# Optimization experiments

Hardware: AMD Instinct MI355X
Metric: run time of the kernel (lower is better)

## Reference

```python
import jax, jax.numpy as jnp
import numpy as np

HIDDEN_DIM = 256
NLAT, NLON = 64, 128
BATCH, N_STATIONS = 2, 1024


def _grid_coords():
    lat = jnp.linspace(-90.0, 90.0, NLAT)
    lon = jnp.linspace(-180.0, 180.0, NLON)
    lat_mesh, lon_mesh = jnp.meshgrid(lat, lon, indexing='ij')
    return lat_mesh.reshape(-1), lon_mesh.reshape(-1)  # (n_grid,)


def setup_inputs() -> dict:
    key = jax.random.key(0)
    k1, k2, k3, k4, k5, k6 = jax.random.split(key, 6)
    station_features = jax.random.normal(k1, (BATCH, N_STATIONS, HIDDEN_DIM), dtype=jnp.float32)
    station_coords = jax.random.normal(k2, (BATCH, N_STATIONS, 3), dtype=jnp.float32)
    mask = jnp.ones((BATCH, N_STATIONS), dtype=jnp.float32)
    # distance_mlp params: Linear(3,32) -> GELU -> Linear(32,1) -> Softplus
    W1 = jax.random.normal(k3, (3, 32), dtype=jnp.float32) * (1.0 / np.sqrt(3.0))
    b1 = jax.random.normal(k4, (32,), dtype=jnp.float32) * 0.02
    W2 = jax.random.normal(k5, (32, 1), dtype=jnp.float32) * (1.0 / np.sqrt(32.0))
    b2 = jax.random.normal(k6, (1,), dtype=jnp.float32) * 0.02
    return {"station_features": station_features, "station_coords": station_coords,
            "mask": mask, "W1": W1, "b1": b1, "W2": W2, "b2": b2}


def reference(station_features, station_coords, mask, W1, b1, W2, b2):
    lat_grid, lon_grid = _grid_coords()  # (G,)
    station_lat = station_coords[:, :, 0]  # (B,S)
    station_lon = station_coords[:, :, 1]
    dlat = station_lat[:, :, None] - lat_grid[None, None, :]  # (B,S,G)
    dlon = station_lon[:, :, None] - lon_grid[None, None, :]
    dist = jnp.sqrt(dlat**2 + dlon**2 + 1e-6)
    dist_features = jnp.stack([dist, dlat, dlon], axis=-1)  # (B,S,G,3)
    h = jax.nn.gelu(dist_features @ W1 + b1, approximate=False)  # (B,S,G,32)
    weights = jax.nn.softplus((h @ W2 + b2)[..., 0])  # (B,S,G)
    weights = weights * mask[:, :, None]
    weights = jax.nn.softmax(weights, axis=1)  # over stations
    grid = jnp.einsum('bsg,bsd->bgd', weights, station_features)
    grid = grid.reshape(station_features.shape[0], NLAT, NLON, HIDDEN_DIM)
    return jnp.transpose(grid, (0, 3, 1, 2))  # (B, D, nlat, nlon)
```

## Files before the change

### kernel.cpp

```cpp
#include <hip/hip_runtime.h>
#include <math.h>

#define NLAT 64
#define NLON 128
#define HID  256
#define NSTA 1024
#define NG   (NLAT * NLON)
#define TG   16
#define SC   128
#define NCH  4
#define NGRP 16
#define TABN 2048
#define TABW 4.5f

#define LOG2E 1.4426950408889634f
#define LN2   0.69314718055994531f

typedef float f32x4 __attribute__((ext_vector_type(4)));
typedef _Float16 f16x8 __attribute__((ext_vector_type(8)));

__device__ __forceinline__ float gelu_ref(float x) {
    const float p  = 0.3275911f;
    const float a1 = 0.254829592f, a2 = -0.284496736f, a3 = 1.421413741f,
                a4 = -1.453152027f, a5 = 1.061405429f;
    float z  = x * 0.70710678118654752f;
    float az = fabsf(z);
    float t  = __builtin_amdgcn_rcpf(fmaf(p, az, 1.0f));
    float poly = fmaf(fmaf(fmaf(fmaf(a5, t, a4), t, a3), t, a2), t, a1) * t;
    float e  = __builtin_amdgcn_exp2f(az * az * -LOG2E);
    float r  = fmaf(-poly, e, 1.0f);
    float erfz = copysignf(r, z);
    float hx = 0.5f * x;
    return fmaf(hx, erfz, hx);
}

__global__ __launch_bounds__(256)
void cvt_kernel(const float* __restrict__ feats,
                const float* __restrict__ W1, const float* __restrict__ b1,
                const float* __restrict__ W2, const float* __restrict__ b2p,
                _Float16* __restrict__ fhi, _Float16* __restrict__ flo,
                float* __restrict__ wbuf) {
    const int blk = blockIdx.x;
    if (blk == 256) {
        if (threadIdx.x == 0) {
            const float ISCALE = (float)TABN / TABW;
            const float CELL   = TABW / (float)TABN;
            float A = 0.0f, B = 0.0f, C = 0.0f, D = b2p[0];
            for (int j = 0; j < 32; ++j) {
                float a = W1[j], b = W1[32 + j], c = W1[64 + j], d = b1[j], w2 = W2[j];
                wbuf[j * 8 + 0] = a * ISCALE;
                wbuf[j * 8 + 1] = b * ISCALE;
                wbuf[j * 8 + 2] = c * ISCALE;
                wbuf[j * 8 + 3] = d * ISCALE;
                wbuf[j * 8 + 4] = w2;
                wbuf[j * 8 + 5] = 0.5f * w2 * CELL;
                wbuf[j * 8 + 6] = 0.0f;
                wbuf[j * 8 + 7] = 0.0f;
                A = fmaf(0.5f * w2, a, A);
                B = fmaf(0.5f * w2, b, B);
                C = fmaf(0.5f * w2, c, C);
                D = fmaf(0.5f * w2, d, D);
            }
            wbuf[256] = A; wbuf[257] = B; wbuf[258] = C; wbuf[259] = D;
        }
        return;
    }
    __shared__ float tile[32][68];
    const int b  = blk >> 7;
    const int st = (blk >> 2) & 31;
    const int dt = blk & 3;
    {
        const int s  = threadIdx.x >> 3;
        const int dq = threadIdx.x & 7;
        const float* src = feats + ((size_t)(b * NSTA + st * 32 + s)) * HID + dt * 64 + dq * 8;
        float4 v0 = *(const float4*)src;
        float4 v1 = *(const float4*)(src + 4);
        *(float4*)&tile[s][dq * 8]     = v0;
        *(float4*)&tile[s][dq * 8 + 4] = v1;
    }
    __syncthreads();
    const int d  = threadIdx.x >> 2;
    const int sq = threadIdx.x & 3;
    f16x8 hi8, lo8;
#pragma unroll
    for (int k = 0; k < 8; ++k) {
        float v = tile[sq * 8 + k][d];
        _Float16 h = (_Float16)v;
        hi8[k] = h;
        lo8[k] = (_Float16)(v - (float)h);
    }
    const size_t o = ((size_t)(b * HID + dt * 64 + d)) * NSTA + st * 32 + sq * 8;
    *(f16x8*)&fhi[o] = hi8;
    *(f16x8*)&flo[o] = lo8;
}

__global__ __launch_bounds__(256, 6)
void s2g_kernel(const float* __restrict__ coords,
                const float* __restrict__ maskp,
                const float* __restrict__ wbuf,
                const _Float16* __restrict__ fhi,
                const _Float16* __restrict__ flo,
                float* __restrict__ out,
                float* __restrict__ acc1,
                float2* __restrict__ ml)
{
    __shared__ float gtab[TABN];
    __shared__ __align__(16) f16x8 fragAh[256];
    __shared__ __align__(16) f16x8 fragAl[256];
    __shared__ __align__(16) float maxbuf[NGRP * TG];
    __shared__ __align__(16) float psum[NGRP * TG];
    __shared__ __align__(16) float mS[TG], lS[TG], alphaS[TG];

    const int tid  = threadIdx.x;
    const int half = blockIdx.x >> 10;
    const int b    = (blockIdx.x >> 9) & 1;
    const int blk  = blockIdx.x & 511;
    const int lat  = blk >> 3;
    const int lon0 = (blk & 7) * TG;
    const int sbase = half * (NSTA / 2);

    const float latv = -90.0f + (180.0f / 63.0f) * (float)lat;
    const float LIM  = (float)TABN - 0.5f;

    const float CELL = TABW / (float)TABN;
#pragma unroll
    for (int k = tid; k < TABN; k += 256) {
        float x = ((float)k + 0.5f) * CELL;
        gtab[k] = gelu_ref(-x);
    }
    if (tid < TG) { mS[tid] = -1.0e30f; lS[tid] = 0.0f; }

    const f32x4 lin = *(const f32x4*)&wbuf[256];

    const int gA   = tid & (TG - 1);
    const int sgrp = tid >> 4;
    const float lonvA = -180.0f + (360.0f / 127.0f) * (float)(lon0 + gA);

    const int lane = tid & 63;
    const int wv   = tid >> 6;

    f32x4 acc[4];
#pragma unroll
    for (int t = 0; t < 4; ++t) acc[t] = (f32x4){0.0f, 0.0f, 0.0f, 0.0f};

    const float* cbase = coords + (size_t)b * NSTA * 3;
    const float* mbase = maskp  + (size_t)b * NSTA;
    const _Float16* fhb = fhi + (size_t)b * HID * NSTA;
    const _Float16* flb = flo + (size_t)b * HID * NSTA;

    __syncthreads();

    for (int c = 0; c < NCH; ++c) {
        const int s0 = sbase + c * SC;

        float dist[8], dlat[8], dlon[8], v[8];
#pragma unroll
        for (int i = 0; i < 8; ++i) {
            const int s = s0 + sgrp * 8 + i;
            float sla = cbase[(size_t)s * 3 + 0];
            float slo = cbase[(size_t)s * 3 + 1];
            float dla = sla - latv;
            float dlo = slo - lonvA;
            dlat[i] = dla;
            dlon[i] = dlo;
            float dss = sqrtf(fmaf(dla, dla, fmaf(dlo, dlo, 1e-6f)));
            dist[i] = dss;
            v[i] = fmaf(lin.x, dss, fmaf(lin.y, dla, fmaf(lin.z, dlo, lin.w)));
        }
#pragma unroll 2
        for (int j = 0; j < 32; ++j) {
            const f32x4 wq = *(const f32x4*)&wbuf[j * 8];
            const float2 wp = *(const float2*)&wbuf[j * 8 + 4];
#pragma unroll
            for (int i = 0; i < 8; ++i) {
                float pre = fmaf(wq.x, dist[i], fmaf(wq.y, dlat[i], fmaf(wq.z, dlon[i], wq.w)));
                v[i] = fmaf(wp.y, fabsf(pre), v[i]);
                float a = fminf(fabsf(pre), LIM);
                v[i] = fmaf(wp.x, gtab[(unsigned)a], v[i]);
            }
        }
        float lmax = -3.0e38f;
#pragma unroll
        for (int i = 0; i < 8; ++i) {
            const int s = s0 + sgrp * 8 + i;
            float x  = v[i];
            float ax = fabsf(x);
            float e  = __builtin_amdgcn_exp2f(-ax * LOG2E);
            float sp = fmaxf(x, 0.0f) + __builtin_amdgcn_logf(1.0f + e) * LN2;
            v[i] = sp * mbase[s];
            lmax = fmaxf(lmax, v[i]);
        }
        maxbuf[sgrp * TG + gA] = lmax;
        __syncthreads();

        if (tid < TG) {
            float cm = maxbuf[tid];
#pragma unroll
            for (int k = 1; k < NGRP; ++k) cm = fmaxf(cm, maxbuf[k * TG + tid]);
            float mold = mS[tid];
            float mnew = fmaxf(mold, cm);
            alphaS[tid] = __builtin_amdgcn_exp2f((mold - mnew) * LOG2E);
            mS[tid] = mnew;
        }
        __syncthreads();

        {
            float m  = mS[gA];
            float ps = 0.0f;
            f16x8 fh, fl;
#pragma unroll
            for (int i = 0; i < 8; ++i) {
                float p = __builtin_amdgcn_exp2f((v[i] - m) * LOG2E);
                _Float16 h = (_Float16)p;
                fh[i] = h;
                fl[i] = (_Float16)(p - (float)h);
                ps += p;
            }
            const int idx = ((sgrp >> 2) << 6) + (((sgrp & 3) << 4) | gA);
            fragAh[idx] = fh;
            fragAl[idx] = fl;
            psum[sgrp * TG + gA] = ps;
        }
        __syncthreads();

        if (tid < TG) {
            float t = 0.0f;
#pragma unroll
            for (int k = 0; k < NGRP; ++k) t += psum[k * TG + tid];
            lS[tid] = lS[tid] * alphaS[tid] + t;
        }

        {
            const f32x4 al = *(const f32x4*)&alphaS[(lane >> 4) * 4];
#pragma unroll
            for (int t = 0; t < 4; ++t) acc[t] = acc[t] * al;

            const int srow = s0 + ((lane >> 4) * 8);
            const int dbase = wv * 64 + (lane & 15);
#pragma unroll
            for (int kc = 0; kc < 4; ++kc) {
                f16x8 ah = fragAh[(kc << 6) + lane];
                f16x8 al16 = fragAl[(kc << 6) + lane];
#pragma unroll
                for (int t = 0; t < 4; ++t) {
                    const size_t off = (size_t)(dbase + t * 16) * NSTA + srow + kc * 32;
                    f16x8 bh = *(const f16x8*)(fhb + off);
                    f16x8 bl = *(const f16x8*)(flb + off);
                    acc[t] = __builtin_amdgcn_mfma_f32_16x16x32_f16(ah, bh, acc[t], 0, 0, 0);
                    acc[t] = __builtin_amdgcn_mfma_f32_16x16x32_f16(ah, bl, acc[t], 0, 0, 0);
                    acc[t] = __builtin_amdgcn_mfma_f32_16x16x32_f16(al16, bh, acc[t], 0, 0, 0);
                }
            }
        }
    }
    __syncthreads();

    {
        float* dst = half ? acc1 : out;
        const int m0 = (lane >> 4) * 4;
        const size_t gbase = (size_t)lat * NLON + lon0 + m0;
#pragma unroll
        for (int t = 0; t < 4; ++t) {
            const int d = wv * 64 + t * 16 + (lane & 15);
            *reinterpret_cast<f32x4*>(dst + ((size_t)(b * HID + d)) * NG + gbase) = acc[t];
        }
        if (tid < TG)
            ml[((half << 1) + b) * NG + lat * NLON + lon0 + tid] = make_float2(mS[tid], lS[tid]);
    }
}

__global__ __launch_bounds__(256)
void comb_kernel(float* __restrict__ out, const float* __restrict__ acc1,
                 const float2* __restrict__ ml) {
    const int x    = blockIdx.x;
    const int b    = x >> 9;
    const int lat  = (x >> 3) & 63;
    const int dseg = x & 7;
    const int lon  = threadIdx.x & 127;
    const int dsub = threadIdx.x >> 7;
    const int g    = lat * NLON + lon;

    const float2 p0 = ml[b * NG + g];
    const float2 p1 = ml[(2 + b) * NG + g];
    const float M  = fmaxf(p0.x, p1.x);
    float s0 = __builtin_amdgcn_exp2f((p0.x - M) * LOG2E);
    float s1 = __builtin_amdgcn_exp2f((p1.x - M) * LOG2E);
    const float rl = 1.0f / fmaf(p0.y, s0, p1.y * s1);
    s0 *= rl; s1 *= rl;

#pragma unroll 4
    for (int k = 0; k < 16; ++k) {
        const int d = dseg * 32 + dsub + k * 2;
        const size_t o = ((size_t)(b * HID + d)) * NG + g;
        out[o] = fmaf(out[o], s0, acc1[o] * s1);
    }
}

extern "C" void kernel_launch(void* const* d_in, const int* in_sizes, int n_in,
                              void* d_out, int out_size, void* d_ws, size_t ws_size,
                              hipStream_t stream) {
    const float* feats  = (const float*)d_in[0];
    const float* coords = (const float*)d_in[1];
    const float* maskp  = (const float*)d_in[2];
    const float* W1     = (const float*)d_in[3];
    const float* b1     = (const float*)d_in[4];
    const float* W2     = (const float*)d_in[5];
    const float* b2     = (const float*)d_in[6];
    float* out          = (float*)d_out;

    _Float16* fhi = (_Float16*)d_ws;
    _Float16* flo = fhi + (size_t)2 * HID * NSTA;
    float*  acc1 = (float*)((char*)d_ws + (size_t)2 * 1048576);
    float2* ml   = (float2*)((char*)d_ws + (size_t)2 * 1048576 + (size_t)2 * HID * NG * 4);
    float*  wbuf = (float*)((char*)d_ws + (size_t)2 * 1048576 + (size_t)2 * HID * NG * 4 + 262144);

    hipLaunchKernelGGL(cvt_kernel, dim3(257), dim3(256), 0, stream,
                       feats, W1, b1, W2, b2, fhi, flo, wbuf);
    hipLaunchKernelGGL(s2g_kernel, dim3(2048), dim3(256), 0, stream,
                       coords, maskp, wbuf, fhi, flo, out, acc1, ml);
    hipLaunchKernelGGL(comb_kernel, dim3(1024), dim3(256), 0, stream, out, acc1, ml);
}
```

Baseline: 271.0 us.

## Split score computation and PV matmul into separate kernels via score buffer

```diff
diff --git a/kernel.cpp b/kernel.cpp
--- a/kernel.cpp
+++ b/kernel.cpp
@@ -12,6 +12,9 @@
 #define NGRP 16
 #define TABN 2048
 #define TABW 4.5f
+#define AG   8
+#define SCA  256
+#define NCHA 4
 
 #define LOG2E 1.4426950408889634f
 #define LN2   0.69314718055994531f
@@ -94,15 +97,209 @@
     *(f16x8*)&flo[o] = lo8;
 }
 
+
+__global__ __launch_bounds__(256, 8)
+void score_kernel(const float* __restrict__ coords,
+                  const float* __restrict__ maskp,
+                  const float* __restrict__ wbuf,
+                  float* __restrict__ sbuf,
+                  float* __restrict__ mout,
+                  float* __restrict__ lout)
+{
+    __shared__ float gtab[TABN];
+    __shared__ float4 wpk[32];
+    __shared__ float2 w2pk[32];
+    __shared__ float wmax[2][4][AG];
+    __shared__ float lred[32][AG];
+
+    const int tid  = threadIdx.x;
+    const int b    = blockIdx.x >> 10;
+    const int tile = blockIdx.x & 1023;
+    const int g0   = tile * AG;
+    const int lat  = g0 >> 7;
+    const float latv = -90.0f + (180.0f / 63.0f) * (float)lat;
+
+    const float CELL = TABW / (float)TABN;
+#pragma unroll
+    for (int k = tid; k < TABN; k += 256) {
+        float x = ((float)k + 0.5f) * CELL;
+        gtab[k] = gelu_ref(-x);
+    }
+    if (tid < 32) {
+        wpk[tid]  = *(const float4*)&wbuf[tid * 8];
+        w2pk[tid] = *(const float2*)&wbuf[tid * 8 + 4];
+    }
+    const f32x4 lin = *(const f32x4*)&wbuf[256];
+    const float LIM = (float)TABN - 0.5f;
+
+    const int gA   = tid & (AG - 1);
+    const int sgrp = tid >> 3;
+    const int lane = tid & 63;
+    const int wv   = tid >> 6;
+    const float lonvA = -180.0f + (360.0f / 127.0f) * (float)((g0 & 127) + gA);
+
+    const float* cbase = coords + (size_t)b * NSTA * 3;
+    const float* mbase = maskp  + (size_t)b * NSTA;
+    float* srow = sbuf + ((size_t)(b * NG + g0 + gA)) * NSTA;
+
+    float m_t = -1.0e30f, l_t = 0.0f;
+    __syncthreads();
+
+    for (int c = 0; c < NCHA; ++c) {
+        const int sb = c * SCA + sgrp * 8;
+
+        float dist[8], dla_[8], dlo_[8], v[8];
+#pragma unroll
+        for (int i = 0; i < 8; ++i) {
+            const int s = sb + i;
+            float sla = cbase[(size_t)s * 3 + 0];
+            float slo = cbase[(size_t)s * 3 + 1];
+            float dla = sla - latv;
+            float dlo = slo - lonvA;
+            dla_[i] = dla;
+            dlo_[i] = dlo;
+            float dss = sqrtf(fmaf(dla, dla, fmaf(dlo, dlo, 1e-6f)));
+            dist[i] = dss;
+            v[i] = fmaf(lin.x, dss, fmaf(lin.y, dla, fmaf(lin.z, dlo, lin.w)));
+        }
+#pragma unroll 2
+        for (int j = 0; j < 32; ++j) {
+            const float4 wq = wpk[j];
+            const float2 wp = w2pk[j];
+#pragma unroll
+            for (int i = 0; i < 8; ++i) {
+                float pre = fmaf(wq.x, dist[i], fmaf(wq.y, dla_[i], fmaf(wq.z, dlo_[i], wq.w)));
+                v[i] = fmaf(wp.y, fabsf(pre), v[i]);
+                float a = fminf(fabsf(pre), LIM);
+                v[i] = fmaf(wp.x, gtab[(unsigned)a], v[i]);
+            }
+        }
+        float lmax = -3.0e38f;
+#pragma unroll
+        for (int i = 0; i < 8; ++i) {
+            float x  = v[i];
+            float ax = fabsf(x);
+            float e  = __builtin_amdgcn_exp2f(-ax * LOG2E);
+            float sp = fmaxf(x, 0.0f) + __builtin_amdgcn_logf(1.0f + e) * LN2;
+            v[i] = sp * mbase[sb + i];
+            lmax = fmaxf(lmax, v[i]);
+        }
+        f32x4 st0 = {v[0], v[1], v[2], v[3]};
+        f32x4 st1 = {v[4], v[5], v[6], v[7]};
+        *(f32x4*)(srow + sb)     = st0;
+        *(f32x4*)(srow + sb + 4) = st1;
+
+        float wm = lmax;
+        wm = fmaxf(wm, __shfl_xor(wm, 8, 64));
+        wm = fmaxf(wm, __shfl_xor(wm, 16, 64));
+        wm = fmaxf(wm, __shfl_xor(wm, 32, 64));
+        if (lane < AG) wmax[c & 1][wv][lane] = wm;
+        __syncthreads();
+
+        float mnew = m_t;
+#pragma unroll
+        for (int w = 0; w < 4; ++w) mnew = fmaxf(mnew, wmax[c & 1][w][gA]);
+        float alpha = __builtin_amdgcn_exp2f((m_t - mnew) * LOG2E);
+        m_t = mnew;
+        float ps = 0.0f;
+#pragma unroll
+        for (int i = 0; i < 8; ++i) ps += __builtin_amdgcn_exp2f((v[i] - mnew) * LOG2E);
+        l_t = l_t * alpha + ps;
+    }
+
+    lred[sgrp][gA] = l_t;
+    __syncthreads();
+    if (tid < AG) {
+        float t = 0.0f;
+#pragma unroll
+        for (int k = 0; k < 32; ++k) t += lred[k][tid];
+        mout[b * NG + g0 + tid] = m_t;
+        lout[b * NG + g0 + tid] = t;
+    }
+}
+
+__global__ __launch_bounds__(256, 4)
+void pv_kernel(const float* __restrict__ sbuf,
+               const float* __restrict__ mout,
+               const float* __restrict__ lout,
+               const _Float16* __restrict__ fhi,
+               const _Float16* __restrict__ flo,
+               float* __restrict__ out)
+{
+    const int b    = blockIdx.x >> 9;
+    const int tile = blockIdx.x & 511;
+    const int g0   = tile * TG;
+    const int tid  = threadIdx.x;
+    const int lane = tid & 63;
+    const int wv   = tid >> 6;
+
+    const int row = lane & 15;
+    const int kg  = lane >> 4;
+    const float mrow = mout[b * NG + g0 + row];
+    const float* srow = sbuf + ((size_t)(b * NG + g0 + row)) * NSTA + kg * 8;
+    const _Float16* fhb = fhi + (size_t)b * HID * NSTA;
+    const _Float16* flb = flo + (size_t)b * HID * NSTA;
+    const int dbase = wv * 64 + row;
+
+    f32x4 acc[4];
+#pragma unroll
+    for (int t = 0; t < 4; ++t) acc[t] = (f32x4){0.0f, 0.0f, 0.0f, 0.0f};
+
+    for (int c = 0; c < 8; ++c) {
+        const int s0 = c * 128;
+#pragma unroll
+        for (int kc = 0; kc < 4; ++kc) {
+            const int k0 = s0 + kc * 32;
+            f32x4 sa = *(const f32x4*)(srow + k0);
+            f32x4 sc = *(const f32x4*)(srow + k0 + 4);
+            f16x8 ah, al;
+#pragma unroll
+            for (int e = 0; e < 4; ++e) {
+                float p = __builtin_amdgcn_exp2f((sa[e] - mrow) * LOG2E);
+                _Float16 h = (_Float16)p;
+                ah[e] = h;
+                al[e] = (_Float16)(p - (float)h);
+            }
+#pragma unroll
+            for (int e = 0; e < 4; ++e) {
+                float p = __builtin_amdgcn_exp2f((sc[e] - mrow) * LOG2E);
+                _Float16 h = (_Float16)p;
+                ah[4 + e] = h;
+                al[4 + e] = (_Float16)(p - (float)h);
+            }
+            const int srw = k0 + kg * 8;
+#pragma unroll
+            for (int t = 0; t < 4; ++t) {
+                const size_t off = (size_t)(dbase + t * 16) * NSTA + srw;
+                f16x8 bh = *(const f16x8*)(fhb + off);
+                f16x8 bl = *(const f16x8*)(flb + off);
+                acc[t] = __builtin_amdgcn_mfma_f32_16x16x32_f16(ah, bh, acc[t], 0, 0, 0);
+                acc[t] = __builtin_amdgcn_mfma_f32_16x16x32_f16(ah, bl, acc[t], 0, 0, 0);
+                acc[t] = __builtin_amdgcn_mfma_f32_16x16x32_f16(al, bh, acc[t], 0, 0, 0);
+            }
+        }
+    }
+    const int m0 = (lane >> 4) * 4;
+    const float4 l4 = *(const float4*)&lout[b * NG + g0 + m0];
+    const float4 rl = make_float4(1.0f / l4.x, 1.0f / l4.y, 1.0f / l4.z, 1.0f / l4.w);
+#pragma unroll
+    for (int t = 0; t < 4; ++t) {
+        const int d = wv * 64 + t * 16 + row;
+        float4 o;
+        o.x = acc[t].x * rl.x;
+        o.y = acc[t].y * rl.y;
+        o.z = acc[t].z * rl.z;
+        o.w = acc[t].w * rl.w;
+        *reinterpret_cast<float4*>(out + ((size_t)(b * HID + d)) * NG + g0 + m0) = o;
+    }
+}
+
+
 __global__ __launch_bounds__(256, 6)
-void s2g_kernel(const float* __restrict__ coords,
-                const float* __restrict__ maskp,
+void s2g_kernel(const float* __restrict__ coords, const float* __restrict__ maskp,
                 const float* __restrict__ wbuf,
-                const _Float16* __restrict__ fhi,
-                const _Float16* __restrict__ flo,
-                float* __restrict__ out,
-                float* __restrict__ acc1,
-                float2* __restrict__ ml)
+                const _Float16* __restrict__ fhi, const _Float16* __restrict__ flo,
+                float* __restrict__ out, float* __restrict__ acc1, float2* __restrict__ ml)
 {
     __shared__ float gtab[TABN];
     __shared__ __align__(16) f16x8 fragAh[256];
@@ -118,10 +315,8 @@
     const int lat  = blk >> 3;
     const int lon0 = (blk & 7) * TG;
     const int sbase = half * (NSTA / 2);
-
     const float latv = -90.0f + (180.0f / 63.0f) * (float)lat;
     const float LIM  = (float)TABN - 0.5f;
-
     const float CELL = TABW / (float)TABN;
 #pragma unroll
     for (int k = tid; k < TABN; k += 256) {
@@ -129,40 +324,29 @@
         gtab[k] = gelu_ref(-x);
     }
     if (tid < TG) { mS[tid] = -1.0e30f; lS[tid] = 0.0f; }
-
     const f32x4 lin = *(const f32x4*)&wbuf[256];
-
     const int gA   = tid & (TG - 1);
     const int sgrp = tid >> 4;
     const float lonvA = -180.0f + (360.0f / 127.0f) * (float)(lon0 + gA);
-
     const int lane = tid & 63;
     const int wv   = tid >> 6;
-
     f32x4 acc[4];
 #pragma unroll
     for (int t = 0; t < 4; ++t) acc[t] = (f32x4){0.0f, 0.0f, 0.0f, 0.0f};
-
     const float* cbase = coords + (size_t)b * NSTA * 3;
     const float* mbase = maskp  + (size_t)b * NSTA;
     const _Float16* fhb = fhi + (size_t)b * HID * NSTA;
     const _Float16* flb = flo + (size_t)b * HID * NSTA;
-
     __syncthreads();
-
     for (int c = 0; c < NCH; ++c) {
         const int s0 = sbase + c * SC;
-
         float dist[8], dlat[8], dlon[8], v[8];
 #pragma unroll
         for (int i = 0; i < 8; ++i) {
             const int s = s0 + sgrp * 8 + i;
-            float sla = cbase[(size_t)s * 3 + 0];
-            float slo = cbase[(size_t)s * 3 + 1];
-            float dla = sla - latv;
-            float dlo = slo - lonvA;
-            dlat[i] = dla;
-            dlon[i] = dlo;
+            float dla = cbase[(size_t)s * 3 + 0] - latv;
+            float dlo = cbase[(size_t)s * 3 + 1] - lonvA;
+            dlat[i] = dla; dlon[i] = dlo;
             float dss = sqrtf(fmaf(dla, dla, fmaf(dlo, dlo, 1e-6f)));
             dist[i] = dss;
             v[i] = fmaf(lin.x, dss, fmaf(lin.y, dla, fmaf(lin.z, dlo, lin.w)));
@@ -192,7 +376,6 @@
         }
         maxbuf[sgrp * TG + gA] = lmax;
         __syncthreads();
-
         if (tid < TG) {
             float cm = maxbuf[tid];
 #pragma unroll
@@ -203,7 +386,6 @@
             mS[tid] = mnew;
         }
         __syncthreads();
-
         {
             float m  = mS[gA];
             float ps = 0.0f;
@@ -222,19 +404,16 @@
             psum[sgrp * TG + gA] = ps;
         }
         __syncthreads();
-
         if (tid < TG) {
             float t = 0.0f;
 #pragma unroll
             for (int k = 0; k < NGRP; ++k) t += psum[k * TG + tid];
             lS[tid] = lS[tid] * alphaS[tid] + t;
         }
-
         {
             const f32x4 al = *(const f32x4*)&alphaS[(lane >> 4) * 4];
 #pragma unroll
             for (int t = 0; t < 4; ++t) acc[t] = acc[t] * al;
-
             const int srow = s0 + ((lane >> 4) * 8);
             const int dbase = wv * 64 + (lane & 15);
 #pragma unroll
@@ -254,7 +433,6 @@
         }
     }
     __syncthreads();
-
     {
         float* dst = half ? acc1 : out;
         const int m0 = (lane >> 4) * 4;
@@ -279,7 +457,6 @@
     const int lon  = threadIdx.x & 127;
     const int dsub = threadIdx.x >> 7;
     const int g    = lat * NLON + lon;
-
     const float2 p0 = ml[b * NG + g];
     const float2 p1 = ml[(2 + b) * NG + g];
     const float M  = fmaxf(p0.x, p1.x);
@@ -287,7 +464,6 @@
     float s1 = __builtin_amdgcn_exp2f((p1.x - M) * LOG2E);
     const float rl = 1.0f / fmaf(p0.y, s0, p1.y * s1);
     s0 *= rl; s1 *= rl;
-
 #pragma unroll 4
     for (int k = 0; k < 16; ++k) {
         const int d = dseg * 32 + dsub + k * 2;
@@ -310,13 +486,32 @@
 
     _Float16* fhi = (_Float16*)d_ws;
     _Float16* flo = fhi + (size_t)2 * HID * NSTA;
-    float*  acc1 = (float*)((char*)d_ws + (size_t)2 * 1048576);
-    float2* ml   = (float2*)((char*)d_ws + (size_t)2 * 1048576 + (size_t)2 * HID * NG * 4);
-    float*  wbuf = (float*)((char*)d_ws + (size_t)2 * 1048576 + (size_t)2 * HID * NG * 4 + 262144);
-
-    hipLaunchKernelGGL(cvt_kernel, dim3(257), dim3(256), 0, stream,
-                       feats, W1, b1, W2, b2, fhi, flo, wbuf);
-    hipLaunchKernelGGL(s2g_kernel, dim3(2048), dim3(256), 0, stream,
-                       coords, maskp, wbuf, fhi, flo, out, acc1, ml);
-    hipLaunchKernelGGL(comb_kernel, dim3(1024), dim3(256), 0, stream, out, acc1, ml);
-}
+
+    const size_t off_sbuf = (size_t)2 << 20;
+    const size_t off_m    = off_sbuf + (size_t)2 * NG * NSTA * 4;
+    const size_t off_l    = off_m + 65536;
+    const size_t off_w    = off_l + 65536;
+    const size_t NEEDED   = off_w + 4096;
+
+    if (ws_size >= NEEDED) {
+        float* sbuf = (float*)((char*)d_ws + off_sbuf);
+        float* mout = (float*)((char*)d_ws + off_m);
+        float* lout = (float*)((char*)d_ws + off_l);
+        float* wbuf = (float*)((char*)d_ws + off_w);
+        hipLaunchKernelGGL(cvt_kernel, dim3(257), dim3(256), 0, stream,
+                           feats, W1, b1, W2, b2, fhi, flo, wbuf);
+        hipLaunchKernelGGL(score_kernel, dim3(2048), dim3(256), 0, stream,
+                           coords, maskp, wbuf, sbuf, mout, lout);
+        hipLaunchKernelGGL(pv_kernel, dim3(1024), dim3(256), 0, stream,
+                           sbuf, mout, lout, fhi, flo, out);
+    } else {
+        float*  acc1 = (float*)((char*)d_ws + (size_t)2 * 1048576);
+        float2* ml   = (float2*)((char*)d_ws + (size_t)2 * 1048576 + (size_t)2 * HID * NG * 4);
+        float*  wbuf = (float*)((char*)d_ws + (size_t)2 * 1048576 + (size_t)2 * HID * NG * 4 + 262144);
+        hipLaunchKernelGGL(cvt_kernel, dim3(257), dim3(256), 0, stream,
+                           feats, W1, b1, W2, b2, fhi, flo, wbuf);
+        hipLaunchKernelGGL(s2g_kernel, dim3(2048), dim3(256), 0, stream,
+                           coords, maskp, wbuf, fhi, flo, out, acc1, ml);
+        hipLaunchKernelGGL(comb_kernel, dim3(1024), dim3(256), 0, stream, out, acc1, ml);
+    }
+}
```

After: 352.1 us. 1.3x slower.

## Skip saturated GELU table lookups and streamline softmax reductions

Applied to the files above, without the earlier changes.

```diff
diff --git a/kernel.cpp b/kernel.cpp
--- a/kernel.cpp
+++ b/kernel.cpp
@@ -9,7 +9,6 @@
 #define TG   16
 #define SC   128
 #define NCH  4
-#define NGRP 16
 #define TABN 2048
 #define TABW 4.5f
 
@@ -45,6 +44,7 @@
         if (threadIdx.x == 0) {
             const float ISCALE = (float)TABN / TABW;
             const float CELL   = TABW / (float)TABN;
+            const float gend   = gelu_ref(-((float)TABN - 0.5f) * CELL);
             float A = 0.0f, B = 0.0f, C = 0.0f, D = b2p[0];
             for (int j = 0; j < 32; ++j) {
                 float a = W1[j], b = W1[32 + j], c = W1[64 + j], d = b1[j], w2 = W2[j];
@@ -60,6 +60,7 @@
                 B = fmaf(0.5f * w2, b, B);
                 C = fmaf(0.5f * w2, c, C);
                 D = fmaf(0.5f * w2, d, D);
+                D = fmaf(w2, gend, D);
             }
             wbuf[256] = A; wbuf[257] = B; wbuf[258] = C; wbuf[259] = D;
         }
@@ -107,9 +108,12 @@
     __shared__ float gtab[TABN];
     __shared__ __align__(16) f16x8 fragAh[256];
     __shared__ __align__(16) f16x8 fragAl[256];
-    __shared__ __align__(16) float maxbuf[NGRP * TG];
-    __shared__ __align__(16) float psum[NGRP * TG];
-    __shared__ __align__(16) float mS[TG], lS[TG], alphaS[TG];
+    __shared__ __align__(16) float4 wpk[32];
+    __shared__ float w2t[32];
+    __shared__ float w2h[32];
+    __shared__ __align__(16) float wmaxW[4][TG];
+    __shared__ __align__(16) float alphaS[TG];
+    __shared__ __align__(16) float lred[TG][TG + 1];
 
     const int tid  = threadIdx.x;
     const int half = blockIdx.x >> 10;
@@ -121,15 +125,19 @@
 
     const float latv = -90.0f + (180.0f / 63.0f) * (float)lat;
     const float LIM  = (float)TABN - 0.5f;
-
     const float CELL = TABW / (float)TABN;
+
+    const float gend = gelu_ref(-LIM * CELL);
 #pragma unroll
     for (int k = tid; k < TABN; k += 256) {
         float x = ((float)k + 0.5f) * CELL;
-        gtab[k] = gelu_ref(-x);
-    }
-    if (tid < TG) { mS[tid] = -1.0e30f; lS[tid] = 0.0f; }
-
+        gtab[k] = gelu_ref(-x) - gend;
+    }
+    if (tid < 32) {
+        wpk[tid] = *(const float4*)&wbuf[tid * 8];
+        w2t[tid] = wbuf[tid * 8 + 4];
+        w2h[tid] = wbuf[tid * 8 + 5];
+    }
     const f32x4 lin = *(const f32x4*)&wbuf[256];
 
     const int gA   = tid & (TG - 1);
@@ -148,35 +156,45 @@
     const _Float16* fhb = fhi + (size_t)b * HID * NSTA;
     const _Float16* flb = flo + (size_t)b * HID * NSTA;
 
+    float m_A = -1.0e30f;
+    float l_t = 0.0f;
+
     __syncthreads();
 
     for (int c = 0; c < NCH; ++c) {
         const int s0 = sbase + c * SC;
 
-        float dist[8], dlat[8], dlon[8], v[8];
+        float dist[8], dla_[8], dlo_[8], v[8];
 #pragma unroll
         for (int i = 0; i < 8; ++i) {
             const int s = s0 + sgrp * 8 + i;
-            float sla = cbase[(size_t)s * 3 + 0];
-            float slo = cbase[(size_t)s * 3 + 1];
-            float dla = sla - latv;
-            float dlo = slo - lonvA;
-            dlat[i] = dla;
-            dlon[i] = dlo;
+            float dla = cbase[(size_t)s * 3 + 0] - latv;
+            float dlo = cbase[(size_t)s * 3 + 1] - lonvA;
+            dla_[i] = dla;
+            dlo_[i] = dlo;
             float dss = sqrtf(fmaf(dla, dla, fmaf(dlo, dlo, 1e-6f)));
             dist[i] = dss;
             v[i] = fmaf(lin.x, dss, fmaf(lin.y, dla, fmaf(lin.z, dlo, lin.w)));
         }
 #pragma unroll 2
         for (int j = 0; j < 32; ++j) {
-            const f32x4 wq = *(const f32x4*)&wbuf[j * 8];
-            const float2 wp = *(const float2*)&wbuf[j * 8 + 4];
+            const float4 wq = wpk[j];
+            const float  wy = w2h[j];
+            float amin = 1.0e30f;
 #pragma unroll
             for (int i = 0; i < 8; ++i) {
-                float pre = fmaf(wq.x, dist[i], fmaf(wq.y, dlat[i], fmaf(wq.z, dlon[i], wq.w)));
-                v[i] = fmaf(wp.y, fabsf(pre), v[i]);
-                float a = fminf(fabsf(pre), LIM);
-                v[i] = fmaf(wp.x, gtab[(unsigned)a], v[i]);
+                float pre = fmaf(wq.x, dist[i], fmaf(wq.y, dla_[i], fmaf(wq.z, dlo_[i], wq.w)));
+                v[i] = fmaf(wy, fabsf(pre), v[i]);
+                amin = fminf(amin, fabsf(pre));
+            }
+            if (__any(amin < LIM)) {
+                const float w2 = w2t[j];
+#pragma unroll
+                for (int i = 0; i < 8; ++i) {
+                    float pre = fmaf(wq.x, dist[i], fmaf(wq.y, dla_[i], fmaf(wq.z, dlo_[i], wq.w)));
+                    float a = fminf(fabsf(pre), LIM);
+                    v[i] = fmaf(w2, gtab[(unsigned)a], v[i]);
+                }
             }
         }
         float lmax = -3.0e38f;
@@ -190,27 +208,25 @@
             v[i] = sp * mbase[s];
             lmax = fmaxf(lmax, v[i]);
         }
-        maxbuf[sgrp * TG + gA] = lmax;
+        float wm = lmax;
+        wm = fmaxf(wm, __shfl_xor(wm, 16, 64));
+        wm = fmaxf(wm, __shfl_xor(wm, 32, 64));
+        if (lane < TG) wmaxW[wv][lane] = wm;
         __syncthreads();
 
-        if (tid < TG) {
-            float cm = maxbuf[tid];
-#pragma unroll
-            for (int k = 1; k < NGRP; ++k) cm = fmaxf(cm, maxbuf[k * TG + tid]);
-            float mold = mS[tid];
-            float mnew = fmaxf(mold, cm);
-            alphaS[tid] = __builtin_amdgcn_exp2f((mold - mnew) * LOG2E);
-            mS[tid] = mnew;
-        }
-        __syncthreads();
+        float cmx = fmaxf(fmaxf(wmaxW[0][gA], wmaxW[1][gA]),
+                          fmaxf(wmaxW[2][gA], wmaxW[3][gA]));
+        float mnew  = fmaxf(m_A, cmx);
+        float alpha = __builtin_amdgcn_exp2f((m_A - mnew) * LOG2E);
+        m_A = mnew;
+        if (tid < TG) alphaS[tid] = alpha;
 
         {
-            float m  = mS[gA];
             float ps = 0.0f;
             f16x8 fh, fl;
 #pragma unroll
             for (int i = 0; i < 8; ++i) {
-                float p = __builtin_amdgcn_exp2f((v[i] - m) * LOG2E);
+                float p = __builtin_amdgcn_exp2f((v[i] - mnew) * LOG2E);
                 _Float16 h = (_Float16)p;
                 fh[i] = h;
                 fl[i] = (_Float16)(p - (float)h);
@@ -219,16 +235,9 @@
             const int idx = ((sgrp >> 2) << 6) + (((sgrp & 3) << 4) | gA);
             fragAh[idx] = fh;
             fragAl[idx] = fl;
-            psum[sgrp * TG + gA] = ps;
+            l_t = fmaf(l_t, alpha, ps);
         }
         __syncthreads();
-
-        if (tid < TG) {
-            float t = 0.0f;
-#pragma unroll
-            for (int k = 0; k < NGRP; ++k) t += psum[k * TG + tid];
-            lS[tid] = lS[tid] * alphaS[tid] + t;
-        }
 
         {
             const f32x4 al = *(const f32x4*)&alphaS[(lane >> 4) * 4];
@@ -253,8 +262,9 @@
             }
         }
     }
+
+    lred[sgrp][gA] = l_t;
     __syncthreads();
-
     {
         float* dst = half ? acc1 : out;
         const int m0 = (lane >> 4) * 4;
@@ -264,8 +274,12 @@
             const int d = wv * 64 + t * 16 + (lane & 15);
             *reinterpret_cast<f32x4*>(dst + ((size_t)(b * HID + d)) * NG + gbase) = acc[t];
         }
-        if (tid < TG)
-            ml[((half << 1) + b) * NG + lat * NLON + lon0 + tid] = make_float2(mS[tid], lS[tid]);
+        if (tid < TG) {
+            float t = 0.0f;
+#pragma unroll
+            for (int k = 0; k < TG; ++k) t += lred[k][tid];
+            ml[((half << 1) + b) * NG + lat * NLON + lon0 + tid] = make_float2(m_A, t);
+        }
     }
 }
 
```

New measurement: 261.3 us. -3.6%, faster.
